# Kernel optimization log

Hardware: AMD Instinct MI355X
Metric: run time of the kernel (lower is better)

Reference implementation:

```python
import jax, jax.numpy as jnp
import numpy as np


def setup_inputs() -> dict:
    key = jax.random.key(0)
    k1, k2, k3, k4, k5 = jax.random.split(key, 5)
    B, Te, Td, H = 16, 256, 128, 512
    return {
        "encoder_out_seq": jax.random.normal(k1, (B, Te, H), dtype=jnp.float32),
        "decoder_out_seq": jax.random.normal(k2, (B, Td, H), dtype=jnp.float32),
        "W_a": jax.random.normal(k3, (H, H), dtype=jnp.float32) * 0.02,
        "U_a": jax.random.normal(k4, (H, H), dtype=jnp.float32) * 0.02,
        "V_a": jax.random.normal(k5, (H, 1), dtype=jnp.float32) * 0.02,
    }


def reference(encoder_out_seq, decoder_out_seq, W_a, U_a, V_a):
    # encoder_out_seq: [B, Te, H], decoder_out_seq: [B, Td, H]
    # Original loops over decoder timesteps via K.rnn; the math per step is
    # independent, so we compute all timesteps at once (same result).
    W_s = jnp.einsum("beh,hk->bek", encoder_out_seq, W_a)      # [B, Te, H]
    U_h = jnp.einsum("bdh,hk->bdk", decoder_out_seq, U_a)      # [B, Td, H]
    # energies: tanh(W_s + U_h) @ V_a -> [B, Td, Te]
    act = jnp.tanh(W_s[:, None, :, :] + U_h[:, :, None, :])     # [B, Td, Te, H]
    e = jnp.einsum("bdeh,h->bde", act, V_a[:, 0])               # [B, Td, Te]
    e = jax.nn.softmax(e, axis=-1)                              # softmax over encoder steps
    # context: sum_e e * enc -> [B, Td, H]
    c = jnp.einsum("bde,beh->bdh", e, encoder_out_seq)
    return (c, e)
```

## Files before the change

### kernel.cpp

```cpp
#include <hip/hip_runtime.h>

#define B_  16
#define TE_ 256
#define TD_ 128
#define H_  512

#define C_TANH 2.88539008177792681472f
#define LOG2E  1.44269504088896340736f

typedef __attribute__((ext_vector_type(8))) short short8v;
typedef __attribute__((ext_vector_type(4))) float floatx4;

__device__ __forceinline__ float wave_sum(float v) {
#pragma unroll
  for (int m = 32; m; m >>= 1) v += __shfl_xor(v, m, 64);
  return v;
}
__device__ __forceinline__ float wave_max(float v) {
#pragma unroll
  for (int m = 32; m; m >>= 1) v = fmaxf(v, __shfl_xor(v, m, 64));
  return v;
}
__device__ __forceinline__ ushort f2bf(float f) {
  unsigned u = __builtin_bit_cast(unsigned, f);
  u += 0x7fffu + ((u >> 16) & 1u);
  return (ushort)(u >> 16);
}
__device__ __forceinline__ float bf2f(ushort u) {
  return __builtin_bit_cast(float, (unsigned)u << 16);
}
__device__ __forceinline__ unsigned pk2(float a, float b) {
  return (unsigned)f2bf(a) | ((unsigned)f2bf(b) << 16);
}

__global__ __launch_bounds__(256) void prep_all(
    const float* __restrict__ enc, const float* __restrict__ dec,
    const float* __restrict__ Wa, const float* __restrict__ Ua,
    ushort* __restrict__ encB, ushort* __restrict__ decB,
    ushort* __restrict__ encT, ushort* __restrict__ WaT,
    ushort* __restrict__ UaT)
{
  __shared__ float tl[32 * 66];
  const int tid = threadIdx.x;
  const int x = blockIdx.x, y = blockIdx.y, z = blockIdx.z;
  const int r = tid >> 3, g = tid & 7;
  const int hh = tid >> 2, tq = tid & 3;

  if (y < 8) {
    const int t0 = y * 32, h0 = x * 64;
    const float* s = enc + ((size_t)z * TE_ + t0) * H_ + h0;
    float4 f0 = *(const float4*)(s + (size_t)r * H_ + g * 8);
    float4 f1 = *(const float4*)(s + (size_t)r * H_ + g * 8 + 4);
    uint4 pk = {pk2(f0.x, f0.y), pk2(f0.z, f0.w), pk2(f1.x, f1.y), pk2(f1.z, f1.w)};
    *(uint4*)(encB + ((size_t)z * TE_ + t0 + r) * H_ + h0 + g * 8) = pk;
    float* t = &tl[r * 66 + g * 8];
    t[0] = f0.x; t[1] = f0.y; t[2] = f0.z; t[3] = f0.w;
    t[4] = f1.x; t[5] = f1.y; t[6] = f1.z; t[7] = f1.w;
    __syncthreads();
    float v[8];
#pragma unroll
    for (int i = 0; i < 8; ++i) v[i] = tl[(tq * 8 + i) * 66 + hh];
    uint4 tp = {pk2(v[0], v[1]), pk2(v[2], v[3]), pk2(v[4], v[5]), pk2(v[6], v[7])};
    *(uint4*)(encT + ((size_t)z * H_ + h0 + hh) * TE_ + t0 + tq * 8) = tp;
  } else if (y < 12) {
    const int t0 = (y - 8) * 32, h0 = x * 64;
    const float* s = dec + ((size_t)z * TD_ + t0) * H_ + h0;
    float4 f0 = *(const float4*)(s + (size_t)r * H_ + g * 8);
    float4 f1 = *(const float4*)(s + (size_t)r * H_ + g * 8 + 4);
    uint4 pk = {pk2(f0.x, f0.y), pk2(f0.z, f0.w), pk2(f1.x, f1.y), pk2(f1.z, f1.w)};
    *(uint4*)(decB + ((size_t)z * TD_ + t0 + r) * H_ + h0 + g * 8) = pk;
  } else {
    const float* s = (y == 12) ? Wa : Ua;
    ushort* d = (y == 12) ? WaT : UaT;
    const int r0 = z * 32, c0 = x * 64;
    float4 f0 = *(const float4*)(s + (size_t)(r0 + r) * H_ + c0 + g * 8);
    float4 f1 = *(const float4*)(s + (size_t)(r0 + r) * H_ + c0 + g * 8 + 4);
    float* t = &tl[r * 66 + g * 8];
    t[0] = f0.x; t[1] = f0.y; t[2] = f0.z; t[3] = f0.w;
    t[4] = f1.x; t[5] = f1.y; t[6] = f1.z; t[7] = f1.w;
    __syncthreads();
    float v[8];
#pragma unroll
    for (int i = 0; i < 8; ++i) v[i] = tl[(tq * 8 + i) * 66 + hh];
    uint4 tp = {pk2(v[0], v[1]), pk2(v[2], v[3]), pk2(v[4], v[5]), pk2(v[6], v[7])};
    *(uint4*)(d + (size_t)(c0 + hh) * H_ + r0 + tq * 8) = tp;
  }
}

__global__ __launch_bounds__(256) void gemm_phaseA(
    const ushort* __restrict__ encB, const ushort* __restrict__ WaT,
    ushort* __restrict__ E_T,
    const ushort* __restrict__ decB, const ushort* __restrict__ UaT,
    float* __restrict__ eU)
{
  __shared__ __attribute__((aligned(16))) ushort As[64 * 40];
  __shared__ __attribute__((aligned(16))) ushort Bs[128 * 40];

  const int tid = threadIdx.x;
  const int l = tid & 63;
  const int w = tid >> 6;
  const int l15 = l & 15, l4 = l >> 4;
  const int id = blockIdx.x;
  const bool isA1 = id < 256;
  int bm, bn;
  const ushort *Ag, *Bg;
  if (isA1) {
    bm = (id >> 5) * 64;
    bn = (id & 31) * 128;
    Ag = WaT + (long)bm * H_;
    Bg = encB + (long)bn * H_;
  } else {
    const int i2 = id - 256;
    bm = (i2 >> 2) * 64;
    bn = (i2 & 3) * 128;
    Ag = decB + (long)bm * H_;
    Bg = UaT + (long)bn * H_;
  }

  const int rowA = tid >> 2, kcA = (tid & 3) << 3;
  short8v aR, bR0, bR1;
  aR  = *(const short8v*)(Ag + (long)rowA * H_ + kcA);
  bR0 = *(const short8v*)(Bg + (long)rowA * H_ + kcA);
  bR1 = *(const short8v*)(Bg + (long)(64 + rowA) * H_ + kcA);

  floatx4 acc[8] = {};

  for (int kt = 0; kt < H_; kt += 32) {
    if (kt) __syncthreads();
    *(short8v*)&As[rowA * 40 + kcA] = aR;
    *(short8v*)&Bs[rowA * 40 + kcA] = bR0;
    *(short8v*)&Bs[(64 + rowA) * 40 + kcA] = bR1;
    __syncthreads();
    if (kt + 32 < H_) {
      aR  = *(const short8v*)(Ag + (long)rowA * H_ + kt + 32 + kcA);
      bR0 = *(const short8v*)(Bg + (long)rowA * H_ + kt + 32 + kcA);
      bR1 = *(const short8v*)(Bg + (long)(64 + rowA) * H_ + kt + 32 + kcA);
    }
    short8v a0 = *(short8v*)&As[(w * 16 + l15) * 40 + l4 * 8];
#pragma unroll
    for (int nt = 0; nt < 8; ++nt) {
      short8v bf = *(short8v*)&Bs[(nt * 16 + l15) * 40 + l4 * 8];
      acc[nt] = __builtin_amdgcn_mfma_f32_16x16x32_bf16(a0, bf, acc[nt], 0, 0, 0);
    }
  }

  const int growb = bm + w * 16 + (l4 << 2);
  if (isA1) {
    const int bb = bn >> 8;
#pragma unroll
    for (int nt = 0; nt < 8; ++nt) {
      const int t = (bn & 255) + nt * 16 + l15;
#pragma unroll
      for (int r = 0; r < 4; ++r) {
        const int h = growb + r;
        E_T[((size_t)bb * H_ + h) * TE_ + t] =
            f2bf(__builtin_amdgcn_exp2f(C_TANH * acc[nt][r]));
      }
    }
  } else {
#pragma unroll
    for (int nt = 0; nt < 8; ++nt) {
      const int gcol = bn + nt * 16 + l15;
#pragma unroll
      for (int r = 0; r < 4; ++r)
        eU[(size_t)(growb + r) * H_ + gcol] =
            __builtin_amdgcn_exp2f(C_TANH * acc[nt][r]);
    }
  }
}

__global__ __launch_bounds__(256) void gemm_ctx(
    const ushort* __restrict__ A, int lda, long sA,
    const ushort* __restrict__ BT, int ldb, long sB,
    float* __restrict__ C, int ldc, long sC, int K)
{
  __shared__ __attribute__((aligned(16))) ushort As[64 * 40];
  __shared__ __attribute__((aligned(16))) ushort Bs[64 * 40];

  const int tid = threadIdx.x;
  const int l = tid & 63;
  const int w = tid >> 6;
  const int l15 = l & 15, l4 = l >> 4;
  const long z = blockIdx.z;
  const int bn = blockIdx.x * 64, bm = blockIdx.y * 64;

  const ushort* Ag = A + z * sA + (long)bm * lda;
  const ushort* Bg = BT + z * sB + (long)bn * ldb;

  const int rowA = tid >> 2, kcA = (tid & 3) << 3;
  short8v aR = *(const short8v*)(Ag + (long)rowA * lda + kcA);
  short8v bR = *(const short8v*)(Bg + (long)rowA * ldb + kcA);

  floatx4 acc[4] = {};

  for (int kt = 0; kt < K; kt += 32) {
    if (kt) __syncthreads();
    *(short8v*)&As[rowA * 40 + kcA] = aR;
    *(short8v*)&Bs[rowA * 40 + kcA] = bR;
    __syncthreads();
    if (kt + 32 < K) {
      aR = *(const short8v*)(Ag + (long)rowA * lda + kt + 32 + kcA);
      bR = *(const short8v*)(Bg + (long)rowA * ldb + kt + 32 + kcA);
    }
    short8v a0 = *(short8v*)&As[(w * 16 + l15) * 40 + l4 * 8];
#pragma unroll
    for (int nt = 0; nt < 4; ++nt) {
      short8v bf = *(short8v*)&Bs[(nt * 16 + l15) * 40 + l4 * 8];
      acc[nt] = __builtin_amdgcn_mfma_f32_16x16x32_bf16(a0, bf, acc[nt], 0, 0, 0);
    }
  }

  const int growb = bm + w * 16 + (l4 << 2);
#pragma unroll
  for (int nt = 0; nt < 4; ++nt) {
    const int gcol = bn + nt * 16 + l15;
#pragma unroll
    for (int r = 0; r < 4; ++r)
      C[z * sC + (long)(growb + r) * ldc + gcol] = acc[nt][r];
  }
}

__global__ __launch_bounds__(512) void energies_softmax(
    const ushort* __restrict__ E_T, const float* __restrict__ eU,
    const float* __restrict__ Va, float* __restrict__ e_out,
    ushort* __restrict__ eB)
{
  __shared__ float part[2][8][TE_];

  const int tid  = threadIdx.x;
  const int lane = tid & 63;
  const int wv   = __builtin_amdgcn_readfirstlane(tid >> 6);
  const int id   = blockIdx.x;
  const int xcd  = id & 7, j = id >> 3;
  const int b    = (xcd << 1) | (j >> 6);
  const int d0   = (j & 63) << 1;

  float4 v0 = *(const float4*)(Va + (lane << 2));
  float4 v1 = *(const float4*)(Va + 256 + (lane << 2));
  const float svtot =
      wave_sum(v0.x + v0.y + v0.z + v0.w + v1.x + v1.y + v1.z + v1.w);

  const float* u0 = eU + (size_t)(b * TD_ + d0 + 0) * H_ + wv * 64;
  const float* u1 = eU + (size_t)(b * TD_ + d0 + 1) * H_ + wv * 64;
  const float* vp = Va + wv * 64;
  const ushort* ep = E_T + ((size_t)(b * H_) + wv * 64) * TE_ + (lane << 2);

  float p0[4] = {}, p1[4] = {};

#pragma unroll 4
  for (int h = 0; h < 64; ++h) {
    const float sV = vp[h];
    const float sU0 = u0[h], sU1 = u1[h];
    ushort4 ew = *(const ushort4*)(ep + (size_t)h * TE_);
    float e0 = bf2f(ew.x), e1 = bf2f(ew.y), e2 = bf2f(ew.z), e3 = bf2f(ew.w);
    p0[0] = fmaf(sV, __builtin_amdgcn_rcpf(fmaf(e0, sU0, 1.f)), p0[0]);
    p0[1] = fmaf(sV, __builtin_amdgcn_rcpf(fmaf(e1, sU0, 1.f)), p0[1]);
    p0[2] = fmaf(sV, __builtin_amdgcn_rcpf(fmaf(e2, sU0, 1.f)), p0[2]);
    p0[3] = fmaf(sV, __builtin_amdgcn_rcpf(fmaf(e3, sU0, 1.f)), p0[3]);
    p1[0] = fmaf(sV, __builtin_amdgcn_rcpf(fmaf(e0, sU1, 1.f)), p1[0]);
    p1[1] = fmaf(sV, __builtin_amdgcn_rcpf(fmaf(e1, sU1, 1.f)), p1[1]);
    p1[2] = fmaf(sV, __builtin_amdgcn_rcpf(fmaf(e2, sU1, 1.f)), p1[2]);
    p1[3] = fmaf(sV, __builtin_amdgcn_rcpf(fmaf(e3, sU1, 1.f)), p1[3]);
  }

  *(float4*)&part[0][wv][lane << 2] = *(float4*)p0;
  *(float4*)&part[1][wv][lane << 2] = *(float4*)p1;
  __syncthreads();

  if (wv < 2) {
    float l4v[4] = {0.f, 0.f, 0.f, 0.f};
#pragma unroll
    for (int w = 0; w < 8; ++w) {
      float4 q = *(const float4*)&part[wv][w][lane << 2];
      l4v[0] += q.x; l4v[1] += q.y; l4v[2] += q.z; l4v[3] += q.w;
    }
#pragma unroll
    for (int q = 0; q < 4; ++q) l4v[q] = svtot - 2.f * l4v[q];
    float m = wave_max(fmaxf(fmaxf(l4v[0], l4v[1]), fmaxf(l4v[2], l4v[3])));
    float p[4];
    float s = 0.f;
#pragma unroll
    for (int q = 0; q < 4; ++q) {
      p[q] = __builtin_amdgcn_exp2f((l4v[q] - m) * LOG2E);
      s += p[q];
    }
    s = wave_sum(s);
    const float inv = 1.0f / s;
    float4 ov = {p[0] * inv, p[1] * inv, p[2] * inv, p[3] * inv};
    const size_t ro = (size_t)(b * TD_ + d0 + wv) * TE_ + (lane << 2);
    *(float4*)(e_out + ro) = ov;
    ushort4 ob = {f2bf(ov.x), f2bf(ov.y), f2bf(ov.z), f2bf(ov.w)};
    *(ushort4*)(eB + ro) = ob;
  }
}

extern "C" void kernel_launch(void* const* d_in, const int* in_sizes, int n_in,
                              void* d_out, int out_size, void* d_ws, size_t ws_size,
                              hipStream_t stream) {
  const float* enc = (const float*)d_in[0];
  const float* dec = (const float*)d_in[1];
  const float* Wa  = (const float*)d_in[2];
  const float* Ua  = (const float*)d_in[3];
  const float* Va  = (const float*)d_in[4];

  float* out_c = (float*)d_out;
  float* out_e = out_c + (size_t)B_ * TD_ * H_;

  char* w8 = (char*)d_ws;
  ushort* E_T  = (ushort*)(w8);
  float*  eU   = (float*)(w8 + (4u << 20));
  ushort* encB = (ushort*)(w8 + (8u << 20));
  ushort* decB = (ushort*)(w8 + (12u << 20));
  ushort* WaT  = (ushort*)(w8 + (14u << 20));
  ushort* UaT  = (ushort*)(w8 + (14u << 20) + (512u << 10));
  ushort* encT = (ushort*)(w8 + (15u << 20));
  ushort* eB   = (ushort*)(w8 + (19u << 20));

  prep_all<<<dim3(8, 14, 16), 256, 0, stream>>>(
      enc, dec, Wa, Ua, encB, decB, encT, WaT, UaT);

  gemm_phaseA<<<384, 256, 0, stream>>>(encB, WaT, E_T, decB, UaT, eU);

  energies_softmax<<<1024, 512, 0, stream>>>(E_T, eU, Va, out_e, eB);

  gemm_ctx<<<dim3(8, 2, 16), 256, 0, stream>>>(
      eB, TE_, (long)TD_ * TE_, encT, TE_, (long)H_ * TE_,
      out_c, H_, (long)TD_ * H_, TE_);
}
```

Measured before the change: 61.36 us.

## Fuse fp32-to-bf16 conversion of enc/dec into phase-A GEMM loads, shrink tiles

The prep kernel no longer writes bf16 copies of the encoder and decoder. The phase-A GEMM now reads fp32 activations directly and converts them to bf16 while staging them into shared memory. The GEMM tile also shrinks from 64x128 to 64x64, doubling the grid to 768 blocks, with a remapped block-index order. This removes one write and one read of the bf16 activation copies, at the cost of fp32 global loads inside the GEMM and less data reuse per tile.

After: 60.48 us. About the same (-1.4%).

```diff
diff --git a/kernel.cpp b/kernel.cpp
--- a/kernel.cpp
+++ b/kernel.cpp
@@ -33,12 +33,10 @@
   return (unsigned)f2bf(a) | ((unsigned)f2bf(b) << 16);
 }
 
-__global__ __launch_bounds__(256) void prep_all(
-    const float* __restrict__ enc, const float* __restrict__ dec,
-    const float* __restrict__ Wa, const float* __restrict__ Ua,
-    ushort* __restrict__ encB, ushort* __restrict__ decB,
-    ushort* __restrict__ encT, ushort* __restrict__ WaT,
-    ushort* __restrict__ UaT)
+__global__ __launch_bounds__(256) void prep_T(
+    const float* __restrict__ enc, const float* __restrict__ Wa,
+    const float* __restrict__ Ua, ushort* __restrict__ encT,
+    ushort* __restrict__ WaT, ushort* __restrict__ UaT)
 {
   __shared__ float tl[32 * 66];
   const int tid = threadIdx.x;
@@ -46,126 +44,139 @@
   const int r = tid >> 3, g = tid & 7;
   const int hh = tid >> 2, tq = tid & 3;
 
+  const float* s;
+  ushort* d;
+  long dstr;
+  int r0, c0;
   if (y < 8) {
-    const int t0 = y * 32, h0 = x * 64;
-    const float* s = enc + ((size_t)z * TE_ + t0) * H_ + h0;
-    float4 f0 = *(const float4*)(s + (size_t)r * H_ + g * 8);
-    float4 f1 = *(const float4*)(s + (size_t)r * H_ + g * 8 + 4);
-    uint4 pk = {pk2(f0.x, f0.y), pk2(f0.z, f0.w), pk2(f1.x, f1.y), pk2(f1.z, f1.w)};
-    *(uint4*)(encB + ((size_t)z * TE_ + t0 + r) * H_ + h0 + g * 8) = pk;
-    float* t = &tl[r * 66 + g * 8];
-    t[0] = f0.x; t[1] = f0.y; t[2] = f0.z; t[3] = f0.w;
-    t[4] = f1.x; t[5] = f1.y; t[6] = f1.z; t[7] = f1.w;
-    __syncthreads();
-    float v[8];
-#pragma unroll
-    for (int i = 0; i < 8; ++i) v[i] = tl[(tq * 8 + i) * 66 + hh];
-    uint4 tp = {pk2(v[0], v[1]), pk2(v[2], v[3]), pk2(v[4], v[5]), pk2(v[6], v[7])};
-    *(uint4*)(encT + ((size_t)z * H_ + h0 + hh) * TE_ + t0 + tq * 8) = tp;
-  } else if (y < 12) {
-    const int t0 = (y - 8) * 32, h0 = x * 64;
-    const float* s = dec + ((size_t)z * TD_ + t0) * H_ + h0;
-    float4 f0 = *(const float4*)(s + (size_t)r * H_ + g * 8);
-    float4 f1 = *(const float4*)(s + (size_t)r * H_ + g * 8 + 4);
-    uint4 pk = {pk2(f0.x, f0.y), pk2(f0.z, f0.w), pk2(f1.x, f1.y), pk2(f1.z, f1.w)};
-    *(uint4*)(decB + ((size_t)z * TD_ + t0 + r) * H_ + h0 + g * 8) = pk;
+    s = enc + (size_t)z * TE_ * H_;
+    d = encT + (size_t)z * H_ * TE_;
+    dstr = TE_;
+    r0 = y * 32; c0 = x * 64;
   } else {
-    const float* s = (y == 12) ? Wa : Ua;
-    ushort* d = (y == 12) ? WaT : UaT;
-    const int r0 = z * 32, c0 = x * 64;
-    float4 f0 = *(const float4*)(s + (size_t)(r0 + r) * H_ + c0 + g * 8);
-    float4 f1 = *(const float4*)(s + (size_t)(r0 + r) * H_ + c0 + g * 8 + 4);
-    float* t = &tl[r * 66 + g * 8];
-    t[0] = f0.x; t[1] = f0.y; t[2] = f0.z; t[3] = f0.w;
-    t[4] = f1.x; t[5] = f1.y; t[6] = f1.z; t[7] = f1.w;
-    __syncthreads();
-    float v[8];
-#pragma unroll
-    for (int i = 0; i < 8; ++i) v[i] = tl[(tq * 8 + i) * 66 + hh];
-    uint4 tp = {pk2(v[0], v[1]), pk2(v[2], v[3]), pk2(v[4], v[5]), pk2(v[6], v[7])};
-    *(uint4*)(d + (size_t)(c0 + hh) * H_ + r0 + tq * 8) = tp;
-  }
-}
-
-__global__ __launch_bounds__(256) void gemm_phaseA(
-    const ushort* __restrict__ encB, const ushort* __restrict__ WaT,
-    ushort* __restrict__ E_T,
-    const ushort* __restrict__ decB, const ushort* __restrict__ UaT,
-    float* __restrict__ eU)
-{
-  __shared__ __attribute__((aligned(16))) ushort As[64 * 40];
-  __shared__ __attribute__((aligned(16))) ushort Bs[128 * 40];
-
+    s = (y == 8) ? Wa : Ua;
+    d = (y == 8) ? WaT : UaT;
+    dstr = H_;
+    r0 = z * 32; c0 = x * 64;
+  }
+
+  float4 f0 = *(const float4*)(s + (size_t)(r0 + r) * H_ + c0 + g * 8);
+  float4 f1 = *(const float4*)(s + (size_t)(r0 + r) * H_ + c0 + g * 8 + 4);
+  float* t = &tl[r * 66 + g * 8];
+  t[0] = f0.x; t[1] = f0.y; t[2] = f0.z; t[3] = f0.w;
+  t[4] = f1.x; t[5] = f1.y; t[6] = f1.z; t[7] = f1.w;
+  __syncthreads();
+  float v[8];
+#pragma unroll
+  for (int i = 0; i < 8; ++i) v[i] = tl[(tq * 8 + i) * 66 + hh];
+  uint4 tp = {pk2(v[0], v[1]), pk2(v[2], v[3]), pk2(v[4], v[5]), pk2(v[6], v[7])};
+  *(uint4*)(d + (size_t)(c0 + hh) * dstr + r0 + tq * 8) = tp;
+}
+
+template <bool CVTA, bool CVTB, int EPI>
+__device__ __forceinline__ void gemm64_body(
+    const void* Asrc, const void* Bsrc, void* dst, int bm, int bn,
+    ushort* As, ushort* Bs)
+{
   const int tid = threadIdx.x;
-  const int l = tid & 63;
-  const int w = tid >> 6;
+  const int l = tid & 63, w = tid >> 6;
   const int l15 = l & 15, l4 = l >> 4;
-  const int id = blockIdx.x;
-  const bool isA1 = id < 256;
-  int bm, bn;
-  const ushort *Ag, *Bg;
-  if (isA1) {
-    bm = (id >> 5) * 64;
-    bn = (id & 31) * 128;
-    Ag = WaT + (long)bm * H_;
-    Bg = encB + (long)bn * H_;
-  } else {
-    const int i2 = id - 256;
-    bm = (i2 >> 2) * 64;
-    bn = (i2 & 3) * 128;
-    Ag = decB + (long)bm * H_;
-    Bg = UaT + (long)bn * H_;
-  }
-
-  const int rowA = tid >> 2, kcA = (tid & 3) << 3;
-  short8v aR, bR0, bR1;
-  aR  = *(const short8v*)(Ag + (long)rowA * H_ + kcA);
-  bR0 = *(const short8v*)(Bg + (long)rowA * H_ + kcA);
-  bR1 = *(const short8v*)(Bg + (long)(64 + rowA) * H_ + kcA);
-
-  floatx4 acc[8] = {};
+  const int rowS = tid >> 2, kc = (tid & 3) << 3;
+
+  const float*  Af = (const float*)Asrc;
+  const ushort* Ab = (const ushort*)Asrc;
+  const float*  Bf = (const float*)Bsrc;
+  const ushort* Bb = (const ushort*)Bsrc;
+  const long arow = (long)(bm * 64 + rowS) * H_ + kc;
+  const long brow = (long)(bn * 64 + rowS) * H_ + kc;
+
+  short8v aR, bR;
+  float4 fa0, fa1, fb0, fb1;
+  if (CVTA) { fa0 = *(const float4*)(Af + arow); fa1 = *(const float4*)(Af + arow + 4); }
+  else      { aR = *(const short8v*)(Ab + arow); }
+  if (CVTB) { fb0 = *(const float4*)(Bf + brow); fb1 = *(const float4*)(Bf + brow + 4); }
+  else      { bR = *(const short8v*)(Bb + brow); }
+
+  floatx4 acc[4] = {};
 
   for (int kt = 0; kt < H_; kt += 32) {
     if (kt) __syncthreads();
-    *(short8v*)&As[rowA * 40 + kcA] = aR;
-    *(short8v*)&Bs[rowA * 40 + kcA] = bR0;
-    *(short8v*)&Bs[(64 + rowA) * 40 + kcA] = bR1;
+    if (CVTA) {
+      uint4 p = {pk2(fa0.x, fa0.y), pk2(fa0.z, fa0.w), pk2(fa1.x, fa1.y), pk2(fa1.z, fa1.w)};
+      *(uint4*)&As[rowS * 40 + kc] = p;
+    } else {
+      *(short8v*)&As[rowS * 40 + kc] = aR;
+    }
+    if (CVTB) {
+      uint4 p = {pk2(fb0.x, fb0.y), pk2(fb0.z, fb0.w), pk2(fb1.x, fb1.y), pk2(fb1.z, fb1.w)};
+      *(uint4*)&Bs[rowS * 40 + kc] = p;
+    } else {
+      *(short8v*)&Bs[rowS * 40 + kc] = bR;
+    }
     __syncthreads();
     if (kt + 32 < H_) {
-      aR  = *(const short8v*)(Ag + (long)rowA * H_ + kt + 32 + kcA);
-      bR0 = *(const short8v*)(Bg + (long)rowA * H_ + kt + 32 + kcA);
-      bR1 = *(const short8v*)(Bg + (long)(64 + rowA) * H_ + kt + 32 + kcA);
+      if (CVTA) { fa0 = *(const float4*)(Af + arow + kt + 32);
+                  fa1 = *(const float4*)(Af + arow + kt + 36); }
+      else      { aR = *(const short8v*)(Ab + arow + kt + 32); }
+      if (CVTB) { fb0 = *(const float4*)(Bf + brow + kt + 32);
+                  fb1 = *(const float4*)(Bf + brow + kt + 36); }
+      else      { bR = *(const short8v*)(Bb + brow + kt + 32); }
     }
     short8v a0 = *(short8v*)&As[(w * 16 + l15) * 40 + l4 * 8];
 #pragma unroll
-    for (int nt = 0; nt < 8; ++nt) {
+    for (int nt = 0; nt < 4; ++nt) {
       short8v bf = *(short8v*)&Bs[(nt * 16 + l15) * 40 + l4 * 8];
       acc[nt] = __builtin_amdgcn_mfma_f32_16x16x32_bf16(a0, bf, acc[nt], 0, 0, 0);
     }
   }
 
-  const int growb = bm + w * 16 + (l4 << 2);
-  if (isA1) {
-    const int bb = bn >> 8;
-#pragma unroll
-    for (int nt = 0; nt < 8; ++nt) {
-      const int t = (bn & 255) + nt * 16 + l15;
-#pragma unroll
-      for (int r = 0; r < 4; ++r) {
-        const int h = growb + r;
-        E_T[((size_t)bb * H_ + h) * TE_ + t] =
+  if (EPI == 0) {
+    ushort* E = (ushort*)dst;
+    const int bb = bn >> 2, t0 = (bn & 3) * 64;
+    const int hb = bm * 64 + w * 16 + (l4 << 2);
+#pragma unroll
+    for (int nt = 0; nt < 4; ++nt) {
+      const int t = t0 + nt * 16 + l15;
+#pragma unroll
+      for (int r = 0; r < 4; ++r)
+        E[((size_t)bb * H_ + hb + r) * TE_ + t] =
             f2bf(__builtin_amdgcn_exp2f(C_TANH * acc[nt][r]));
-      }
     }
   } else {
-#pragma unroll
-    for (int nt = 0; nt < 8; ++nt) {
-      const int gcol = bn + nt * 16 + l15;
+    float* U = (float*)dst;
+    const int growb = bm * 64 + w * 16 + (l4 << 2);
+#pragma unroll
+    for (int nt = 0; nt < 4; ++nt) {
+      const int gcol = bn * 64 + nt * 16 + l15;
 #pragma unroll
       for (int r = 0; r < 4; ++r)
-        eU[(size_t)(growb + r) * H_ + gcol] =
+        U[(size_t)(growb + r) * H_ + gcol] =
             __builtin_amdgcn_exp2f(C_TANH * acc[nt][r]);
     }
+  }
+}
+
+__global__ __launch_bounds__(256) void gemm_phaseA(
+    const float* __restrict__ enc, const ushort* __restrict__ WaT,
+    ushort* __restrict__ E_T,
+    const float* __restrict__ dec, const ushort* __restrict__ UaT,
+    float* __restrict__ eU)
+{
+  __shared__ __attribute__((aligned(16))) ushort As[64 * 40];
+  __shared__ __attribute__((aligned(16))) ushort Bs[64 * 40];
+
+  const int id = blockIdx.x;
+  if (id < 512) {
+    const int x = id & 7, k = id >> 3;
+    const int bm = k & 7;
+    const int bn = x * 8 + (k >> 3);
+    gemm64_body<false, true, 0>(WaT, enc, E_T, bm, bn, As, Bs);
+  } else {
+    const int i2 = id - 512;
+    const int x = i2 & 7, k = i2 >> 3;
+    const int bm = x * 4 + (k & 3);
+    const int bn = k >> 2;
+    gemm64_body<true, false, 1>(dec, UaT, eU, bm, bn, As, Bs);
   }
 }
 
@@ -309,17 +320,14 @@
   char* w8 = (char*)d_ws;
   ushort* E_T  = (ushort*)(w8);
   float*  eU   = (float*)(w8 + (4u << 20));
-  ushort* encB = (ushort*)(w8 + (8u << 20));
-  ushort* decB = (ushort*)(w8 + (12u << 20));
-  ushort* WaT  = (ushort*)(w8 + (14u << 20));
-  ushort* UaT  = (ushort*)(w8 + (14u << 20) + (512u << 10));
-  ushort* encT = (ushort*)(w8 + (15u << 20));
-  ushort* eB   = (ushort*)(w8 + (19u << 20));
-
-  prep_all<<<dim3(8, 14, 16), 256, 0, stream>>>(
-      enc, dec, Wa, Ua, encB, decB, encT, WaT, UaT);
-
-  gemm_phaseA<<<384, 256, 0, stream>>>(encB, WaT, E_T, decB, UaT, eU);
+  ushort* WaT  = (ushort*)(w8 + (8u << 20));
+  ushort* UaT  = (ushort*)(w8 + (8u << 20) + (512u << 10));
+  ushort* encT = (ushort*)(w8 + (9u << 20));
+  ushort* eB   = (ushort*)(w8 + (13u << 20));
+
+  prep_T<<<dim3(8, 10, 16), 256, 0, stream>>>(enc, Wa, Ua, encT, WaT, UaT);
+
+  gemm_phaseA<<<768, 256, 0, stream>>>(enc, WaT, E_T, dec, UaT, eU);
 
   energies_softmax<<<1024, 512, 0, stream>>>(E_T, eU, Va, out_e, eB);
 
```
